# Optimization experiments

Measured on AMD Instinct MI355X. Metric: run time of the kernel, lower is better.

The kernel has to match this reference:

```python
import jax, jax.numpy as jnp
import numpy as np

H_DIM = 1024
N_LAYERS = 2
N_OBJ = 64
BATCH = 512


def setup_inputs() -> dict:
    key = jax.random.key(0)
    k1, k2, k3, k4, k5, k6 = jax.random.split(key, 6)
    return {
        "obj_embed": jax.random.normal(k1, (BATCH, N_OBJ, H_DIM), dtype=jnp.float32),
        "h": jax.random.normal(k2, (1, BATCH, H_DIM), dtype=jnp.float32),
        "zeros_object": jax.random.uniform(k3, (N_OBJ, BATCH), dtype=jnp.float32),
        "t": 0,
        "W_w": jax.random.normal(k4, (H_DIM, N_LAYERS), dtype=jnp.float32) * 0.5,
        "W_ua": jax.random.normal(k5, (H_DIM, H_DIM), dtype=jnp.float32) * 0.01,
        "b_a": jnp.zeros((H_DIM,), dtype=jnp.float32),
        "W_wa": jax.random.normal(k6, (H_DIM, H_DIM), dtype=jnp.float32) * 0.01,
    }


def reference(obj_embed, h, zeros_object, t, W_w, W_ua, b_a, W_wa):
    # obj_embed: (B, n_obj, h_dim) -> (n_obj, B, h_dim)
    oe = jnp.transpose(obj_embed, (1, 0, 2))
    # image_part: (n_obj, B, h_dim)
    image_part = jnp.einsum("obh,hk->obk", oe, W_ua) + b_a
    # h: (1, B, h_dim) -> (B, 1, h_dim); d: (B, 1, h_dim)
    d = jnp.einsum("bsh,hk->bsk", jnp.transpose(h, (1, 0, 2)), W_wa)
    # broadcast (1, B, h_dim) against (n_obj, B, h_dim)
    e = jnp.tanh(jnp.transpose(d, (1, 0, 2)) + image_part)
    # scores: (n_obj, B) = sum over n_layers of e @ W_w
    scores = jnp.einsum("obh,hl->ob", e, W_w)
    alphas = jax.nn.softmax(scores, axis=0) * zeros_object * 10.0
    # weighted sum over objects -> (B, h_dim) -> (B, 1, h_dim)
    out = jnp.einsum("ob,obh->bh", alphas, oe)
    return out[:, None, :]
```

## Files before the change

kernel.cpp:

```cpp
#include <hip/hip_runtime.h>
#include <math.h>

#define H_DIM 1024
#define BATCH 512
#define NOBJ  64
#define M_TOT (NOBJ * BATCH)
#define BK 64

typedef __attribute__((ext_vector_type(8))) _Float16 half8;
typedef __attribute__((ext_vector_type(4))) float f32x4;

__device__ __forceinline__ float fast_tanh(float x) {
    float e = __expf(2.0f * x);
    return 1.0f - __fdividef(2.0f, e + 1.0f);
}

__global__ __launch_bounds__(256) void k0_prep(const float* __restrict__ Wua,
                                               const float* __restrict__ Ww,
                                               _Float16* __restrict__ Wh,
                                               float* __restrict__ wsum) {
    if (blockIdx.x == 0 && blockIdx.y == 0) {
        for (int i = threadIdx.x; i < H_DIM; i += 256)
            wsum[i] = Ww[i * 2] + Ww[i * 2 + 1];
    }
    __shared__ float t[32][33];
    const int k0 = blockIdx.x * 32, n0 = blockIdx.y * 32;
    const int tx = threadIdx.x & 31, ty = threadIdx.x >> 5;
    #pragma unroll
    for (int r = 0; r < 32; r += 8)
        t[ty + r][tx] = Wua[(size_t)(k0 + ty + r) * H_DIM + n0 + tx];
    __syncthreads();
    #pragma unroll
    for (int r = 0; r < 32; r += 8)
        Wh[(size_t)(n0 + ty + r) * H_DIM + k0 + tx] = (_Float16)t[tx][ty + r];
}

__global__ __launch_bounds__(256) void k1_dproj(const float* __restrict__ hmat,
                                                const float* __restrict__ Wwa,
                                                const float* __restrict__ ba,
                                                float* __restrict__ d2) {
    __shared__ float As[32][32];
    __shared__ float Ws[32][64];
    const int tid = threadIdx.x;
    const int m0 = blockIdx.x * 32;
    const int n0 = blockIdx.y * 64;
    const int kbase = blockIdx.z * 256;
    const int ty = tid >> 5;
    const int tx = tid & 31;
    float acc[4][2] = {};

    for (int kc = 0; kc < 256; kc += 32) {
        const int k0 = kbase + kc;
        {
            int m = tid & 31, ks = tid >> 5;
            const float4 v = *(const float4*)&hmat[(size_t)(m0 + m) * H_DIM + k0 + ks * 4];
            As[ks * 4 + 0][m] = v.x;
            As[ks * 4 + 1][m] = v.y;
            As[ks * 4 + 2][m] = v.z;
            As[ks * 4 + 3][m] = v.w;
        }
        {
            #pragma unroll
            for (int l = 0; l < 2; ++l) {
                int u = tid + l * 256;
                int n4 = u & 15, kk = u >> 4;
                *(float4*)&Ws[kk][n4 * 4] =
                    *(const float4*)&Wwa[(size_t)(k0 + kk) * H_DIM + n0 + n4 * 4];
            }
        }
        __syncthreads();
        #pragma unroll
        for (int kk = 0; kk < 32; ++kk) {
            float av[4], bv[2];
            *(float4*)&av[0] = *(const float4*)&As[kk][ty * 4];
            bv[0] = Ws[kk][tx * 2];
            bv[1] = Ws[kk][tx * 2 + 1];
            #pragma unroll
            for (int i = 0; i < 4; ++i)
                #pragma unroll
                for (int j = 0; j < 2; ++j)
                    acc[i][j] += av[i] * bv[j];
        }
        __syncthreads();
    }
    #pragma unroll
    for (int i = 0; i < 4; ++i) {
        int r = m0 + ty * 4 + i;
        #pragma unroll
        for (int j = 0; j < 2; ++j) {
            int c = n0 + tx * 2 + j;
            float v = acc[i][j] + (blockIdx.z == 0 ? ba[c] : 0.0f);
            atomicAdd(&d2[(size_t)r * H_DIM + c], v);
        }
    }
}

__global__ __launch_bounds__(256) void k2_scores(const float* __restrict__ obj,
                                                 const _Float16* __restrict__ Wh,
                                                 const float* __restrict__ d2,
                                                 const float* __restrict__ wsum,
                                                 float* __restrict__ scores) {
    __shared__ _Float16 Asm[128 * BK];
    __shared__ _Float16 Bsm[128 * BK];

    const int hw = blockIdx.x;
    const int x  = hw & 7;
    const int j  = hw >> 3;
    const int m0 = (x * 32 + (j >> 3)) * 128;
    const int n0 = (j & 7) * 128;
    const int tid  = threadIdx.x;
    const int lane = tid & 63;
    const int wid  = tid >> 6;
    const int wr   = wid >> 1, wc = wid & 1;
    const int r    = lane & 15;
    const int g    = lane >> 4;

    const int srow = tid >> 3;
    const int su   = tid & 7;

    f32x4 acc[4][4];
    #pragma unroll
    for (int i = 0; i < 4; ++i)
        #pragma unroll
        for (int jj = 0; jj < 4; ++jj)
            acc[i][jj] = (f32x4){0.f, 0.f, 0.f, 0.f};

    for (int kk0 = 0; kk0 < H_DIM; kk0 += BK) {
        #pragma unroll
        for (int l = 0; l < 4; ++l) {
            const int row = l * 32 + srow;
            const int swz = (su ^ (row & 7)) * 8;
            {
                const int m = m0 + row;
                const size_t base = ((size_t)(m & (BATCH - 1)) * NOBJ + (m >> 9)) * H_DIM
                                    + kk0 + su * 8;
                const float4 v0 = *(const float4*)&obj[base];
                const float4 v1 = *(const float4*)&obj[base + 4];
                half8 w;
                w[0] = (_Float16)v0.x; w[1] = (_Float16)v0.y;
                w[2] = (_Float16)v0.z; w[3] = (_Float16)v0.w;
                w[4] = (_Float16)v1.x; w[5] = (_Float16)v1.y;
                w[6] = (_Float16)v1.z; w[7] = (_Float16)v1.w;
                *(half8*)&Asm[row * 64 + swz] = w;
            }
            {
                const half8 w = *(const half8*)&Wh[(size_t)(n0 + row) * H_DIM + kk0 + su * 8];
                *(half8*)&Bsm[row * 64 + swz] = w;
            }
        }
        __syncthreads();

        #pragma unroll
        for (int s = 0; s < 2; ++s) {
            const int swz = ((s * 4 + g) ^ (r & 7)) * 8;
            half8 a[4], b[4];
            #pragma unroll
            for (int mi = 0; mi < 4; ++mi) {
                const int arow = wr * 64 + mi * 16 + r;
                a[mi] = *(const half8*)&Asm[arow * 64 + swz];
            }
            #pragma unroll
            for (int ni = 0; ni < 4; ++ni) {
                const int brow = wc * 64 + ni * 16 + r;
                b[ni] = *(const half8*)&Bsm[brow * 64 + swz];
            }
            #pragma unroll
            for (int mi = 0; mi < 4; ++mi)
                #pragma unroll
                for (int ni = 0; ni < 4; ++ni)
                    acc[mi][ni] = __builtin_amdgcn_mfma_f32_16x16x32_f16(
                        a[mi], b[ni], acc[mi][ni], 0, 0, 0);
        }
        __syncthreads();
    }

    float wv[4];
    int   col[4];
    #pragma unroll
    for (int ni = 0; ni < 4; ++ni) {
        col[ni] = n0 + wc * 64 + ni * 16 + r;
        wv[ni]  = wsum[col[ni]];
    }
    #pragma unroll
    for (int mi = 0; mi < 4; ++mi) {
        #pragma unroll
        for (int reg = 0; reg < 4; ++reg) {
            const int row = m0 + wr * 64 + mi * 16 + g * 4 + reg;
            const int b   = row & (BATCH - 1);
            const float* d2b = d2 + (size_t)b * H_DIM;
            float part = 0.f;
            #pragma unroll
            for (int ni = 0; ni < 4; ++ni)
                part += fast_tanh(acc[mi][ni][reg] + d2b[col[ni]]) * wv[ni];
            part += __shfl_xor(part, 1);
            part += __shfl_xor(part, 2);
            part += __shfl_xor(part, 4);
            part += __shfl_xor(part, 8);
            if (r == 0) atomicAdd(&scores[row], part);
        }
    }
}

__global__ __launch_bounds__(128) void k3_out(const float* __restrict__ obj,
                                              const float* __restrict__ scores,
                                              const float* __restrict__ zobj,
                                              float* __restrict__ out) {
    __shared__ float sc[NOBJ];
    __shared__ float al[NOBJ];
    const int b = blockIdx.x;
    const int tid = threadIdx.x;
    if (tid < NOBJ) sc[tid] = scores[(size_t)tid * BATCH + b];
    __syncthreads();
    float mx = -1e30f;
    #pragma unroll 8
    for (int o = 0; o < NOBJ; ++o) mx = fmaxf(mx, sc[o]);
    float s = 0.f;
    #pragma unroll 8
    for (int o = 0; o < NOBJ; ++o) s += expf(sc[o] - mx);
    if (tid < NOBJ)
        al[tid] = expf(sc[tid] - mx) / s * zobj[(size_t)tid * BATCH + b] * 10.0f;
    __syncthreads();

    const int h0 = (blockIdx.y * 128 + tid) * 4;
    float4 o4 = {0.f, 0.f, 0.f, 0.f};
    const float* base = obj + (size_t)b * NOBJ * H_DIM + h0;
    #pragma unroll 8
    for (int o = 0; o < NOBJ; ++o) {
        float a = al[o];
        float4 v = *(const float4*)&base[(size_t)o * H_DIM];
        o4.x += a * v.x;
        o4.y += a * v.y;
        o4.z += a * v.z;
        o4.w += a * v.w;
    }
    *(float4*)&out[(size_t)b * H_DIM + h0] = o4;
}

extern "C" void kernel_launch(void* const* d_in, const int* in_sizes, int n_in,
                              void* d_out, int out_size, void* d_ws, size_t ws_size,
                              hipStream_t stream) {
    const float* obj  = (const float*)d_in[0];
    const float* hmat = (const float*)d_in[1];
    const float* zobj = (const float*)d_in[2];
    const float* Ww   = (const float*)d_in[4];
    const float* Wua  = (const float*)d_in[5];
    const float* ba   = (const float*)d_in[6];
    const float* Wwa  = (const float*)d_in[7];
    float* out = (float*)d_out;

    char* ws = (char*)d_ws;
    float*     d2     = (float*)(ws);
    float*     scores = (float*)(ws + (size_t)BATCH * H_DIM * 4);
    float*     wsum   = (float*)(ws + (size_t)BATCH * H_DIM * 4 + (size_t)M_TOT * 4);
    _Float16*  Wh     = (_Float16*)(ws + (size_t)BATCH * H_DIM * 4
                                    + (size_t)M_TOT * 4 + H_DIM * 4);

    hipMemsetAsync(d2, 0, (size_t)BATCH * H_DIM * sizeof(float), stream);
    hipMemsetAsync(scores, 0, (size_t)M_TOT * sizeof(float), stream);

    k0_prep<<<dim3(H_DIM / 32, H_DIM / 32), 256, 0, stream>>>(Wua, Ww, Wh, wsum);
    k1_dproj<<<dim3(BATCH / 32, H_DIM / 64, 4), 256, 0, stream>>>(hmat, Wwa, ba, d2);
    k2_scores<<<dim3((M_TOT / 128) * (H_DIM / 128)), 256, 0, stream>>>(obj, Wh, d2, wsum, scores);
    k3_out<<<dim3(BATCH, 2), 128, 0, stream>>>(obj, scores, zobj, out);
}
```

Measured before the change: 416.7 us.

## Pre-convert object embeddings to fp16 and load GEMM tiles directly into LDS

Adds a conversion pass that writes obj_embed as fp16 to workspace. The score GEMM then streams tiles with global_load_lds instead of register-staged conversion, and the output kernel reads half the bytes. Also removes split-K atomics in the d projection and widens the weight transpose tiles. This costs an extra full pass over the embeddings and workspace space, and the output reduction now uses fp16-rounded embeddings. The old path is kept as a fallback when workspace is too small.

```diff
diff --git a/kernel.cpp b/kernel.cpp
--- a/kernel.cpp
+++ b/kernel.cpp
@@ -10,9 +10,34 @@
 typedef __attribute__((ext_vector_type(8))) _Float16 half8;
 typedef __attribute__((ext_vector_type(4))) float f32x4;
 
+#define GLOAD16(gp, lp) \
+    __builtin_amdgcn_global_load_lds( \
+        (__attribute__((address_space(1))) const unsigned int*)(gp), \
+        (__attribute__((address_space(3))) unsigned int*)(lp), 16, 0, 0)
+
 __device__ __forceinline__ float fast_tanh(float x) {
     float e = __expf(2.0f * x);
     return 1.0f - __fdividef(2.0f, e + 1.0f);
+}
+
+__global__ __launch_bounds__(256) void kA_cvt(const float* __restrict__ obj,
+                                              _Float16* __restrict__ A16) {
+    const size_t i0 = ((size_t)blockIdx.x * 256 + threadIdx.x) * 16;
+    const float4 v0 = *(const float4*)&obj[i0];
+    const float4 v1 = *(const float4*)&obj[i0 + 4];
+    const float4 v2 = *(const float4*)&obj[i0 + 8];
+    const float4 v3 = *(const float4*)&obj[i0 + 12];
+    half8 w0, w1;
+    w0[0] = (_Float16)v0.x; w0[1] = (_Float16)v0.y;
+    w0[2] = (_Float16)v0.z; w0[3] = (_Float16)v0.w;
+    w0[4] = (_Float16)v1.x; w0[5] = (_Float16)v1.y;
+    w0[6] = (_Float16)v1.z; w0[7] = (_Float16)v1.w;
+    w1[0] = (_Float16)v2.x; w1[1] = (_Float16)v2.y;
+    w1[2] = (_Float16)v2.z; w1[3] = (_Float16)v2.w;
+    w1[4] = (_Float16)v3.x; w1[5] = (_Float16)v3.y;
+    w1[6] = (_Float16)v3.z; w1[7] = (_Float16)v3.w;
+    *(half8*)&A16[i0]     = w0;
+    *(half8*)&A16[i0 + 8] = w1;
 }
 
 __global__ __launch_bounds__(256) void k0_prep(const float* __restrict__ Wua,
@@ -23,16 +48,24 @@
         for (int i = threadIdx.x; i < H_DIM; i += 256)
             wsum[i] = Ww[i * 2] + Ww[i * 2 + 1];
     }
-    __shared__ float t[32][33];
-    const int k0 = blockIdx.x * 32, n0 = blockIdx.y * 32;
-    const int tx = threadIdx.x & 31, ty = threadIdx.x >> 5;
-    #pragma unroll
-    for (int r = 0; r < 32; r += 8)
-        t[ty + r][tx] = Wua[(size_t)(k0 + ty + r) * H_DIM + n0 + tx];
+    __shared__ float t[64][65];
+    const int k0 = blockIdx.x * 64, n0 = blockIdx.y * 64;
+    #pragma unroll
+    for (int it = 0; it < 4; ++it) {
+        int idx = it * 256 + threadIdx.x;
+        int kr = idx >> 4, nc = (idx & 15) * 4;
+        *(float4*)&t[kr][nc] = *(const float4*)&Wua[(size_t)(k0 + kr) * H_DIM + n0 + nc];
+    }
     __syncthreads();
     #pragma unroll
-    for (int r = 0; r < 32; r += 8)
-        Wh[(size_t)(n0 + ty + r) * H_DIM + k0 + tx] = (_Float16)t[tx][ty + r];
+    for (int it = 0; it < 2; ++it) {
+        int u = it * 256 + threadIdx.x;
+        int nr = u >> 3, ku = (u & 7) * 8;
+        half8 w;
+        #pragma unroll
+        for (int j = 0; j < 8; ++j) w[j] = (_Float16)t[ku + j][nr];
+        *(half8*)&Wh[(size_t)(n0 + nr) * H_DIM + k0 + ku] = w;
+    }
 }
 
 __global__ __launch_bounds__(256) void k1_dproj(const float* __restrict__ hmat,
@@ -44,13 +77,11 @@
     const int tid = threadIdx.x;
     const int m0 = blockIdx.x * 32;
     const int n0 = blockIdx.y * 64;
-    const int kbase = blockIdx.z * 256;
     const int ty = tid >> 5;
     const int tx = tid & 31;
     float acc[4][2] = {};
 
-    for (int kc = 0; kc < 256; kc += 32) {
-        const int k0 = kbase + kc;
+    for (int k0 = 0; k0 < H_DIM; k0 += 32) {
         {
             int m = tid & 31, ks = tid >> 5;
             const float4 v = *(const float4*)&hmat[(size_t)(m0 + m) * H_DIM + k0 + ks * 4];
@@ -59,14 +90,12 @@
             As[ks * 4 + 2][m] = v.z;
             As[ks * 4 + 3][m] = v.w;
         }
-        {
-            #pragma unroll
-            for (int l = 0; l < 2; ++l) {
-                int u = tid + l * 256;
-                int n4 = u & 15, kk = u >> 4;
-                *(float4*)&Ws[kk][n4 * 4] =
-                    *(const float4*)&Wwa[(size_t)(k0 + kk) * H_DIM + n0 + n4 * 4];
-            }
+        #pragma unroll
+        for (int l = 0; l < 2; ++l) {
+            int u = tid + l * 256;
+            int n4 = u & 15, kk = u >> 4;
+            *(float4*)&Ws[kk][n4 * 4] =
+                *(const float4*)&Wwa[(size_t)(k0 + kk) * H_DIM + n0 + n4 * 4];
         }
         __syncthreads();
         #pragma unroll
@@ -89,13 +118,12 @@
         #pragma unroll
         for (int j = 0; j < 2; ++j) {
             int c = n0 + tx * 2 + j;
-            float v = acc[i][j] + (blockIdx.z == 0 ? ba[c] : 0.0f);
-            atomicAdd(&d2[(size_t)r * H_DIM + c], v);
-        }
-    }
-}
-
-__global__ __launch_bounds__(256) void k2_scores(const float* __restrict__ obj,
+            d2[(size_t)r * H_DIM + c] = acc[i][j] + ba[c];
+        }
+    }
+}
+
+__global__ __launch_bounds__(256) void k2_scores(const _Float16* __restrict__ A16,
                                                  const _Float16* __restrict__ Wh,
                                                  const float* __restrict__ d2,
                                                  const float* __restrict__ wsum,
@@ -115,6 +143,135 @@
     const int r    = lane & 15;
     const int g    = lane >> 4;
 
+    const _Float16* aS[4];
+    const _Float16* bS[4];
+    #pragma unroll
+    for (int c = 0; c < 4; ++c) {
+        const int row = wid * 32 + c * 8 + (lane >> 3);
+        const int u   = lane & 7;
+        const int us  = (u ^ (row & 7)) * 8;
+        const int m   = m0 + row;
+        aS[c] = A16 + ((size_t)(m & (BATCH - 1)) * NOBJ + (m >> 9)) * H_DIM + us;
+        bS[c] = Wh + (size_t)(n0 + row) * H_DIM + us;
+    }
+
+    f32x4 acc[4][4];
+    #pragma unroll
+    for (int i = 0; i < 4; ++i)
+        #pragma unroll
+        for (int jj = 0; jj < 4; ++jj)
+            acc[i][jj] = (f32x4){0.f, 0.f, 0.f, 0.f};
+
+    for (int kk0 = 0; kk0 < H_DIM; kk0 += BK) {
+        #pragma unroll
+        for (int c = 0; c < 4; ++c) {
+            GLOAD16(aS[c] + kk0, &Asm[(wid * 32 + c * 8) * 64]);
+            GLOAD16(bS[c] + kk0, &Bsm[(wid * 32 + c * 8) * 64]);
+        }
+        __syncthreads();
+
+        #pragma unroll
+        for (int s = 0; s < 2; ++s) {
+            const int swz = ((s * 4 + g) ^ (r & 7)) * 8;
+            half8 a[4], b[4];
+            #pragma unroll
+            for (int mi = 0; mi < 4; ++mi)
+                a[mi] = *(const half8*)&Asm[(wr * 64 + mi * 16 + r) * 64 + swz];
+            #pragma unroll
+            for (int ni = 0; ni < 4; ++ni)
+                b[ni] = *(const half8*)&Bsm[(wc * 64 + ni * 16 + r) * 64 + swz];
+            #pragma unroll
+            for (int mi = 0; mi < 4; ++mi)
+                #pragma unroll
+                for (int ni = 0; ni < 4; ++ni)
+                    acc[mi][ni] = __builtin_amdgcn_mfma_f32_16x16x32_f16(
+                        a[mi], b[ni], acc[mi][ni], 0, 0, 0);
+        }
+        __syncthreads();
+    }
+
+    float wv[4];
+    int   col[4];
+    #pragma unroll
+    for (int ni = 0; ni < 4; ++ni) {
+        col[ni] = n0 + wc * 64 + ni * 16 + r;
+        wv[ni]  = wsum[col[ni]];
+    }
+    #pragma unroll
+    for (int mi = 0; mi < 4; ++mi) {
+        #pragma unroll
+        for (int reg = 0; reg < 4; ++reg) {
+            const int row = m0 + wr * 64 + mi * 16 + g * 4 + reg;
+            const int b   = row & (BATCH - 1);
+            const float* d2b = d2 + (size_t)b * H_DIM;
+            float part = 0.f;
+            #pragma unroll
+            for (int ni = 0; ni < 4; ++ni)
+                part += fast_tanh(acc[mi][ni][reg] + d2b[col[ni]]) * wv[ni];
+            part += __shfl_xor(part, 1);
+            part += __shfl_xor(part, 2);
+            part += __shfl_xor(part, 4);
+            part += __shfl_xor(part, 8);
+            if (r == 0) atomicAdd(&scores[row], part);
+        }
+    }
+}
+
+__global__ __launch_bounds__(128) void k3_out16(const _Float16* __restrict__ A16,
+                                                const float* __restrict__ scores,
+                                                const float* __restrict__ zobj,
+                                                float* __restrict__ out) {
+    __shared__ float sc[NOBJ];
+    __shared__ float al[NOBJ];
+    const int b = blockIdx.x;
+    const int tid = threadIdx.x;
+    if (tid < NOBJ) sc[tid] = scores[(size_t)tid * BATCH + b];
+    __syncthreads();
+    float mx = -1e30f;
+    #pragma unroll 8
+    for (int o = 0; o < NOBJ; ++o) mx = fmaxf(mx, sc[o]);
+    float s = 0.f;
+    #pragma unroll 8
+    for (int o = 0; o < NOBJ; ++o) s += expf(sc[o] - mx);
+    if (tid < NOBJ)
+        al[tid] = expf(sc[tid] - mx) / s * zobj[(size_t)tid * BATCH + b] * 10.0f;
+    __syncthreads();
+
+    const int h0 = tid * 8;
+    float a0 = 0, a1 = 0, a2 = 0, a3 = 0, a4 = 0, a5 = 0, a6 = 0, a7 = 0;
+    const _Float16* base = A16 + (size_t)b * NOBJ * H_DIM + h0;
+    #pragma unroll 8
+    for (int o = 0; o < NOBJ; ++o) {
+        float a = al[o];
+        const half8 v = *(const half8*)&base[(size_t)o * H_DIM];
+        a0 += a * (float)v[0]; a1 += a * (float)v[1];
+        a2 += a * (float)v[2]; a3 += a * (float)v[3];
+        a4 += a * (float)v[4]; a5 += a * (float)v[5];
+        a6 += a * (float)v[6]; a7 += a * (float)v[7];
+    }
+    float4 o0 = {a0, a1, a2, a3}, o1 = {a4, a5, a6, a7};
+    *(float4*)&out[(size_t)b * H_DIM + h0]     = o0;
+    *(float4*)&out[(size_t)b * H_DIM + h0 + 4] = o1;
+}
+
+__global__ __launch_bounds__(256) void k2_reg(const float* __restrict__ obj,
+                                              const _Float16* __restrict__ Wh,
+                                              const float* __restrict__ d2,
+                                              const float* __restrict__ wsum,
+                                              float* __restrict__ scores) {
+    __shared__ _Float16 Asm[128 * BK];
+    __shared__ _Float16 Bsm[128 * BK];
+    const int hw = blockIdx.x;
+    const int x  = hw & 7;
+    const int j  = hw >> 3;
+    const int m0 = (x * 32 + (j >> 3)) * 128;
+    const int n0 = (j & 7) * 128;
+    const int tid  = threadIdx.x;
+    const int lane = tid & 63;
+    const int wid  = tid >> 6;
+    const int wr   = wid >> 1, wc = wid & 1;
+    const int r    = lane & 15;
+    const int g    = lane >> 4;
     const int srow = tid >> 3;
     const int su   = tid & 7;
 
@@ -149,21 +306,16 @@
             }
         }
         __syncthreads();
-
         #pragma unroll
         for (int s = 0; s < 2; ++s) {
             const int swz = ((s * 4 + g) ^ (r & 7)) * 8;
             half8 a[4], b[4];
             #pragma unroll
-            for (int mi = 0; mi < 4; ++mi) {
-                const int arow = wr * 64 + mi * 16 + r;
-                a[mi] = *(const half8*)&Asm[arow * 64 + swz];
-            }
-            #pragma unroll
-            for (int ni = 0; ni < 4; ++ni) {
-                const int brow = wc * 64 + ni * 16 + r;
-                b[ni] = *(const half8*)&Bsm[brow * 64 + swz];
-            }
+            for (int mi = 0; mi < 4; ++mi)
+                a[mi] = *(const half8*)&Asm[(wr * 64 + mi * 16 + r) * 64 + swz];
+            #pragma unroll
+            for (int ni = 0; ni < 4; ++ni)
+                b[ni] = *(const half8*)&Bsm[(wc * 64 + ni * 16 + r) * 64 + swz];
             #pragma unroll
             for (int mi = 0; mi < 4; ++mi)
                 #pragma unroll
@@ -201,10 +353,10 @@
     }
 }
 
-__global__ __launch_bounds__(128) void k3_out(const float* __restrict__ obj,
-                                              const float* __restrict__ scores,
-                                              const float* __restrict__ zobj,
-                                              float* __restrict__ out) {
+__global__ __launch_bounds__(128) void k3_out32(const float* __restrict__ obj,
+                                                const float* __restrict__ scores,
+                                                const float* __restrict__ zobj,
+                                                float* __restrict__ out) {
     __shared__ float sc[NOBJ];
     __shared__ float al[NOBJ];
     const int b = blockIdx.x;
@@ -249,17 +401,32 @@
     float* out = (float*)d_out;
 
     char* ws = (char*)d_ws;
-    float*     d2     = (float*)(ws);
-    float*     scores = (float*)(ws + (size_t)BATCH * H_DIM * 4);
-    float*     wsum   = (float*)(ws + (size_t)BATCH * H_DIM * 4 + (size_t)M_TOT * 4);
-    _Float16*  Wh     = (_Float16*)(ws + (size_t)BATCH * H_DIM * 4
-                                    + (size_t)M_TOT * 4 + H_DIM * 4);
-
-    hipMemsetAsync(d2, 0, (size_t)BATCH * H_DIM * sizeof(float), stream);
+    const size_t d2_off     = 0;
+    const size_t scores_off = d2_off + (size_t)BATCH * H_DIM * 4;
+    const size_t wsum_off   = scores_off + (size_t)M_TOT * 4;
+    const size_t Wh_off     = wsum_off + 4096;
+    const size_t A16_off    = Wh_off + (size_t)H_DIM * H_DIM * 2;
+    const size_t need       = A16_off + (size_t)M_TOT * H_DIM * 2;
+
+    float*    d2     = (float*)(ws + d2_off);
+    float*    scores = (float*)(ws + scores_off);
+    float*    wsum   = (float*)(ws + wsum_off);
+    _Float16* Wh     = (_Float16*)(ws + Wh_off);
+    _Float16* A16    = (_Float16*)(ws + A16_off);
+
     hipMemsetAsync(scores, 0, (size_t)M_TOT * sizeof(float), stream);
 
-    k0_prep<<<dim3(H_DIM / 32, H_DIM / 32), 256, 0, stream>>>(Wua, Ww, Wh, wsum);
-    k1_dproj<<<dim3(BATCH / 32, H_DIM / 64, 4), 256, 0, stream>>>(hmat, Wwa, ba, d2);
-    k2_scores<<<dim3((M_TOT / 128) * (H_DIM / 128)), 256, 0, stream>>>(obj, Wh, d2, wsum, scores);
-    k3_out<<<dim3(BATCH, 2), 128, 0, stream>>>(obj, scores, zobj, out);
-}
+    k0_prep<<<dim3(H_DIM / 64, H_DIM / 64), 256, 0, stream>>>(Wua, Ww, Wh, wsum);
+    k1_dproj<<<dim3(BATCH / 32, H_DIM / 64), 256, 0, stream>>>(hmat, Wwa, ba, d2);
+
+    if (ws_size >= need) {
+        kA_cvt<<<dim3(8192), 256, 0, stream>>>(obj, A16);
+        k2_scores<<<dim3((M_TOT / 128) * (H_DIM / 128)), 256, 0, stream>>>(
+            A16, Wh, d2, wsum, scores);
+        k3_out16<<<dim3(BATCH), 128, 0, stream>>>(A16, scores, zobj, out);
+    } else {
+        k2_reg<<<dim3((M_TOT / 128) * (H_DIM / 128)), 256, 0, stream>>>(
+            obj, Wh, d2, wsum, scores);
+        k3_out32<<<dim3(BATCH, 2), 128, 0, stream>>>(obj, scores, zobj, out);
+    }
+}
```

After: 381.9 us. 1.09x faster.
